# Optimization experiments

Measured on AMD Instinct MI355X. Metric: run time of the kernel, lower is better.

## Reference

```python
import jax, jax.numpy as jnp
import numpy as np

B, L, H, P = 4, 4096, 1024, 256


def _bin_op(ei, ej):
    A_i, Bu_i = ei
    A_j, Bu_j = ej
    return (A_j * A_i, A_j * Bu_i + Bu_j)


def _s5(x, log_real, imag, B_real, B_imag, C_real, C_imag, D, log_Delta):
    Lam = jax.lax.complex(-jnp.exp(log_real), imag)                 # [P]
    B_tilde = jax.lax.complex(B_real, B_imag)                        # [P,H]
    C_tilde = jax.lax.complex(C_real, C_imag)                        # [H,P]
    Delta = jnp.exp(log_Delta)                                       # [P]
    Lambda_bar = jnp.exp(Lam * Delta)                                # [P]
    Lam_safe = jnp.where(jnp.abs(Lam) < 1e-6,
                         jnp.full_like(Lam, 1e-6), Lam)
    B_bar = ((Lambda_bar - 1.0) / Lam_safe)[:, None] * B_tilde       # [P,H]
    Bu = x.astype(jnp.complex64) @ B_bar.T                           # [B,L,P]
    La = jnp.broadcast_to(Lambda_bar[None, None, :], Bu.shape)
    _, xs = jax.lax.associative_scan(_bin_op, (La, Bu), axis=1)      # [B,L,P]
    ys = jnp.real(xs @ C_tilde.T) + D * x                            # [B,L,H]
    return jax.nn.gelu(ys, approximate=False)


def setup_inputs() -> dict:
    key = jax.random.key(0)
    ks = jax.random.split(key, 17)
    std_b = 1.0 / H ** 0.5
    std_c = 1.0 / P ** 0.5
    d = {"x": jax.random.normal(ks[0], (B, L, H), dtype=jnp.float32)}
    for i, pfx in enumerate(["fwd", "bwd"]):
        o = 1 + 8 * i
        d[pfx + "_log_real"] = jax.random.normal(ks[o], (P,)) * 0.5
        d[pfx + "_imag"] = jax.random.normal(ks[o + 1], (P,))
        d[pfx + "_B_real"] = jax.random.normal(ks[o + 2], (P, H)) * std_b
        d[pfx + "_B_imag"] = jax.random.normal(ks[o + 3], (P, H)) * std_b
        d[pfx + "_C_real"] = jax.random.normal(ks[o + 4], (H, P)) * std_c
        d[pfx + "_C_imag"] = jax.random.normal(ks[o + 5], (H, P)) * std_c
        d[pfx + "_D"] = jnp.ones((H,), dtype=jnp.float32)
        d[pfx + "_log_Delta"] = jnp.zeros((P,), dtype=jnp.float32)
    return d


def reference(x,
              fwd_log_real, fwd_imag, fwd_B_real, fwd_B_imag,
              fwd_C_real, fwd_C_imag, fwd_D, fwd_log_Delta,
              bwd_log_real, bwd_imag, bwd_B_real, bwd_B_imag,
              bwd_C_real, bwd_C_imag, bwd_D, bwd_log_Delta):
    y_f = _s5(x, fwd_log_real, fwd_imag, fwd_B_real, fwd_B_imag,
              fwd_C_real, fwd_C_imag, fwd_D, fwd_log_Delta)
    x_flip = jnp.flip(x, axis=1)
    y_b = _s5(x_flip, bwd_log_real, bwd_imag, bwd_B_real, bwd_B_imag,
              bwd_C_real, bwd_C_imag, bwd_D, bwd_log_Delta)
    return y_f + jnp.flip(y_b, axis=1)
```

## Files before the change

kernel.cpp:

```cpp
#include <hip/hip_runtime.h>
#include <math.h>


typedef short bf16x8 __attribute__((ext_vector_type(8)));
typedef float f32x4 __attribute__((ext_vector_type(4)));
typedef unsigned short u16x8 __attribute__((ext_vector_type(8)));

__device__ __forceinline__ unsigned short f2bf(float f) {
  union { float f; unsigned int u; } v; v.f = f;
  unsigned int r = (v.u + 0x7FFFu + ((v.u >> 16) & 1u)) >> 16;
  return (unsigned short)r;
}
__device__ __forceinline__ float bf2f(unsigned short s) {
  union { unsigned int u; float f; } v; v.u = ((unsigned int)s) << 16;
  return v.f;
}
__device__ __forceinline__ float gelu_fast(float v) {
  const float u = 1.5957691216057308f * fmaf(0.044715f * v, v * v, v);
  return v / (1.f + __expf(-u));
}
__device__ __forceinline__ void gload16(const unsigned short* g, void* l) {
  __builtin_amdgcn_global_load_lds(
      (const __attribute__((address_space(1))) void*)g,
      (__attribute__((address_space(3))) void*)l, 16, 0, 0);
}

__global__ __launch_bounds__(256) void cast_x_kernel(
    const float* __restrict__ x, unsigned short* __restrict__ xbf) {
  const size_t i = (size_t)blockIdx.x * 256 + threadIdx.x;
  const float4* xv = (const float4*)x;
  float4 a = xv[2 * i], b = xv[2 * i + 1];
  u16x8 r;
  r[0] = f2bf(a.x); r[1] = f2bf(a.y); r[2] = f2bf(a.z); r[3] = f2bf(a.w);
  r[4] = f2bf(b.x); r[5] = f2bf(b.y); r[6] = f2bf(b.z); r[7] = f2bf(b.w);
  *(u16x8*)(xbf + 8 * i) = r;
}

__global__ __launch_bounds__(256) void prep_kernel(
    const float* __restrict__ flr, const float* __restrict__ fim,
    const float* __restrict__ fBr, const float* __restrict__ fBi,
    const float* __restrict__ fCr, const float* __restrict__ fCi,
    const float* __restrict__ flD,
    const float* __restrict__ blr, const float* __restrict__ bim,
    const float* __restrict__ bBr, const float* __restrict__ bBi,
    const float* __restrict__ bCr, const float* __restrict__ bCi,
    const float* __restrict__ blD,
    unsigned short* __restrict__ W, unsigned short* __restrict__ CmT,
    float4* __restrict__ lamp) {
  const int bid = blockIdx.x, tid = threadIdx.x;
  if (bid < 512) {
    const int dir = bid >> 8, p = bid & 255;
    const float* lr_ = dir ? blr : flr;
    const float* im_ = dir ? bim : fim;
    const float* lD_ = dir ? blD : flD;
    const float* Br_ = dir ? bBr : fBr;
    const float* Bi_ = dir ? bBi : fBi;
    const float Lre = -expf(lr_[p]);
    const float Lim = im_[p];
    const float Dl = expf(lD_[p]);
    const float ar = Lre * Dl, ai = Lim * Dl;
    const float er = expf(ar);
    const float lre = er * cosf(ai), lim = er * sinf(ai);
    const float e64 = expf(64.f * ar);
    const float l64re = e64 * cosf(64.f * ai), l64im = e64 * sinf(64.f * ai);
    float sre = Lre, sim = Lim;
    if (sqrtf(Lre * Lre + Lim * Lim) < 1e-6f) { sre = 1e-6f; sim = 0.f; }
    const float den = sre * sre + sim * sim;
    const float fre = ((lre - 1.f) * sre + lim * sim) / den;
    const float fi2 = (lim * sre - (lre - 1.f) * sim) / den;
    if (tid == 0) lamp[dir * 256 + p] = make_float4(lre, lim, l64re, l64im);
    const size_t rowR = (size_t)(dir * 512 + 2 * p) * 1024;
    const size_t rowI = rowR + 1024;
    for (int h = tid; h < 1024; h += 256) {
      const float Br = Br_[p * 1024 + h], Bi = Bi_[p * 1024 + h];
      W[rowR + h] = f2bf(fre * Br - fi2 * Bi);
      W[rowI + h] = f2bf(fre * Bi + fi2 * Br);
    }
  } else {
    const int h = bid - 512;
    for (int k = tid; k < 1024; k += 256) {
      const int dir = k >> 9, within = k & 511;
      const int p = within >> 1, comp = within & 1;
      const float* C = comp ? (dir ? bCi : fCi) : (dir ? bCr : fCr);
      float v = C[(size_t)h * 256 + p];
      if (comp) v = -v;
      CmT[(size_t)h * 1024 + k] = f2bf(v);
    }
  }
}

#define GEMM_KSTEP(ACC, KT, APTR, BPTR)                                        \
  {                                                                            \
    const int k0 = (KT) << 6;                                                  \
    _Pragma("unroll") for (int i = 0; i < 4; ++i) {                            \
      const int r = (i << 5) + tr;                                             \
      const int o = (i << 12) + (tid << 4);                                    \
      gload16(APTR + (size_t)(m0 + r) * 1024 + (k0 + csw), (char*)As + o);     \
      gload16(BPTR + (size_t)(n0 + r) * 1024 + (k0 + csw), (char*)Bs + o);     \
    }                                                                          \
    __syncthreads();                                                           \
    _Pragma("unroll") for (int kk = 0; kk < 64; kk += 32) {                    \
      bf16x8 af[4], bf_[4];                                                    \
      _Pragma("unroll") for (int m4 = 0; m4 < 4; ++m4) {                       \
        const int row = (wm << 6) + (m4 << 4) + fr;                            \
        af[m4] = *(const bf16x8*)&As[row * 64 + ((kk + ks) ^ sw)];             \
      }                                                                        \
      _Pragma("unroll") for (int n4 = 0; n4 < 4; ++n4) {                       \
        const int row = (wn << 6) + (n4 << 4) + fr;                            \
        bf_[n4] = *(const bf16x8*)&Bs[row * 64 + ((kk + ks) ^ sw)];            \
      }                                                                        \
      _Pragma("unroll") for (int m4 = 0; m4 < 4; ++m4)                         \
          _Pragma("unroll") for (int n4 = 0; n4 < 4; ++n4)                     \
              ACC[m4][n4] = __builtin_amdgcn_mfma_f32_16x16x32_bf16(           \
                  af[m4], bf_[n4], ACC[m4][n4], 0, 0, 0);                      \
    }                                                                          \
    __syncthreads();                                                           \
  }

__global__ __launch_bounds__(256) void gemm1_kernel(
    const unsigned short* __restrict__ xbf, const unsigned short* __restrict__ W,
    unsigned short* __restrict__ Zb) {
  __shared__ unsigned short As[128 * 64];
  __shared__ unsigned short Bs[128 * 64];
  const int tid = threadIdx.x;
  const int lane = tid & 63;
  const int w = tid >> 6;
  const int wm = w >> 1, wn = w & 1;
  const int fr = lane & 15;
  const int ks = (lane >> 4) << 3;
  const int sw = (fr & 7) << 3;
  const int tr = tid >> 3;
  const int csw = ((tid & 7) ^ (tr & 7)) << 3;
  const int bsw = ((blockIdx.x & 7) << 7) + (blockIdx.x >> 3);
  const int nt = bsw & 7, mt = bsw >> 3;
  const int m0 = mt << 7, n0 = nt << 7;

  f32x4 acc[4][4] = {};

  for (int kt = 0; kt < 16; ++kt) GEMM_KSTEP(acc, kt, xbf, W);

  const int rb = (lane >> 4) << 2;
#pragma unroll
  for (int m4 = 0; m4 < 4; ++m4)
#pragma unroll
    for (int n4 = 0; n4 < 4; ++n4) {
      const size_t gn = n0 + (wn << 6) + (n4 << 4) + fr;
#pragma unroll
      for (int r = 0; r < 4; ++r) {
        const size_t gm = m0 + (wm << 6) + (m4 << 4) + rb + r;
        Zb[gm * 1024 + gn] = f2bf(acc[m4][n4][r]);
      }
    }
}

__global__ __launch_bounds__(256) void scanA_kernel(
    unsigned int* __restrict__ Zp, const float4* __restrict__ lamp,
    float2* __restrict__ partials) {
  const int p = threadIdx.x;
  const int chunk = blockIdx.x & 63;
  const int dir = (blockIdx.x >> 6) & 1;
  const int b = blockIdx.x >> 7;
  const float4 lp = lamp[dir * 256 + p];
  const float lre = lp.x, lim = lp.y;
  const size_t col = (size_t)dir * 256 + p;
  const size_t mbase = (size_t)b * 4096 + (size_t)chunk * 64;
  float sre = 0.f, sim = 0.f;
  if (dir == 0) {
    for (int i = 0; i < 64; ++i) {
      const size_t idx = (mbase + i) * 512 + col;
      const unsigned int u = Zp[idx];
      const float ur = bf2f((unsigned short)u), ui = bf2f((unsigned short)(u >> 16));
      const float nr = fmaf(lre, sre, fmaf(-lim, sim, ur));
      const float ni = fmaf(lre, sim, fmaf(lim, sre, ui));
      sre = nr; sim = ni;
      Zp[idx] = (unsigned int)f2bf(sre) | ((unsigned int)f2bf(sim) << 16);
    }
  } else {
    for (int i = 63; i >= 0; --i) {
      const size_t idx = (mbase + i) * 512 + col;
      const unsigned int u = Zp[idx];
      const float ur = bf2f((unsigned short)u), ui = bf2f((unsigned short)(u >> 16));
      const float nr = fmaf(lre, sre, fmaf(-lim, sim, ur));
      const float ni = fmaf(lre, sim, fmaf(lim, sre, ui));
      sre = nr; sim = ni;
      Zp[idx] = (unsigned int)f2bf(sre) | ((unsigned int)f2bf(sim) << 16);
    }
  }
  partials[((size_t)(b * 2 + dir) * 256 + p) * 64 + chunk] = make_float2(sre, sim);
}

__global__ __launch_bounds__(256) void scanB_kernel(
    const float2* __restrict__ partials, float2* __restrict__ carries,
    const float4* __restrict__ lamp) {
  const int t = blockIdx.x * 256 + threadIdx.x;
  const int p = t & 255;
  const int dir = (t >> 8) & 1;
  const int b = t >> 9;
  const float4 lp = lamp[dir * 256 + p];
  const float ar = lp.z, ai = lp.w;
  const size_t base = ((size_t)(b * 2 + dir) * 256 + p) * 64;
  float cr = 0.f, ci = 0.f;
  if (dir == 0) {
    for (int c = 0; c < 64; ++c) {
      carries[base + c] = make_float2(cr, ci);
      float2 s = partials[base + c];
      float nr = fmaf(ar, cr, fmaf(-ai, ci, s.x));
      float ni = fmaf(ar, ci, fmaf(ai, cr, s.y));
      cr = nr; ci = ni;
    }
  } else {
    for (int c = 63; c >= 0; --c) {
      carries[base + c] = make_float2(cr, ci);
      float2 s = partials[base + c];
      float nr = fmaf(ar, cr, fmaf(-ai, ci, s.x));
      float ni = fmaf(ar, ci, fmaf(ai, cr, s.y));
      cr = nr; ci = ni;
    }
  }
}

__global__ __launch_bounds__(256) void scanC_kernel(
    const unsigned int* __restrict__ Zp, const float4* __restrict__ lamp,
    const float2* __restrict__ carries, unsigned int* __restrict__ xsbf) {
  const int p = threadIdx.x;
  const int chunk = blockIdx.x & 63;
  const int dir = (blockIdx.x >> 6) & 1;
  const int b = blockIdx.x >> 7;
  const float4 lp = lamp[dir * 256 + p];
  const float lre = lp.x, lim = lp.y;
  const size_t col = (size_t)dir * 256 + p;
  const size_t mbase = (size_t)b * 4096 + (size_t)chunk * 64;
  const float2 K = carries[((size_t)(b * 2 + dir) * 256 + p) * 64 + chunk];
  float qr = lre * K.x - lim * K.y;
  float qi = lre * K.y + lim * K.x;
  if (dir == 0) {
    for (int i = 0; i < 64; ++i) {
      const size_t idx = (mbase + i) * 512 + col;
      const unsigned int u = Zp[idx];
      const float vr = bf2f((unsigned short)u) + qr;
      const float vi = bf2f((unsigned short)(u >> 16)) + qi;
      xsbf[idx] = (unsigned int)f2bf(vr) | ((unsigned int)f2bf(vi) << 16);
      const float t2 = lre * qr - lim * qi;
      qi = lre * qi + lim * qr; qr = t2;
    }
  } else {
    for (int i = 63; i >= 0; --i) {
      const size_t idx = (mbase + i) * 512 + col;
      const unsigned int u = Zp[idx];
      const float vr = bf2f((unsigned short)u) + qr;
      const float vi = bf2f((unsigned short)(u >> 16)) + qi;
      xsbf[idx] = (unsigned int)f2bf(vr) | ((unsigned int)f2bf(vi) << 16);
      const float t2 = lre * qr - lim * qi;
      qi = lre * qi + lim * qr; qr = t2;
    }
  }
}

__global__ __launch_bounds__(256, 2) void gemm2_kernel(
    const unsigned short* __restrict__ A2, const unsigned short* __restrict__ CmT,
    const unsigned short* __restrict__ xbf, const float* __restrict__ Df,
    const float* __restrict__ Db, float* __restrict__ out) {
  __shared__ unsigned short As[128 * 64];
  __shared__ unsigned short Bs[128 * 64];
  const int tid = threadIdx.x;
  const int lane = tid & 63;
  const int w = tid >> 6;
  const int wm = w >> 1, wn = w & 1;
  const int fr = lane & 15;
  const int ks = (lane >> 4) << 3;
  const int sw = (fr & 7) << 3;
  const int tr = tid >> 3;
  const int csw = ((tid & 7) ^ (tr & 7)) << 3;
  const int bsw = ((blockIdx.x & 7) << 7) + (blockIdx.x >> 3);
  const int nt = bsw & 7, mt = bsw >> 3;
  const int m0 = mt << 7, n0 = nt << 7;

  f32x4 accf[4][4] = {};
  f32x4 accb[4][4] = {};

  for (int kt = 0; kt < 8; ++kt) GEMM_KSTEP(accf, kt, A2, CmT);
  for (int kt = 8; kt < 16; ++kt) GEMM_KSTEP(accb, kt, A2, CmT);

  const int rb = (lane >> 4) << 2;
#pragma unroll
  for (int n4 = 0; n4 < 4; ++n4) {
    const size_t gn = n0 + (wn << 6) + (n4 << 4) + fr;
    const float dfv = Df[gn], dbv = Db[gn];
#pragma unroll
    for (int m4 = 0; m4 < 4; ++m4) {
#pragma unroll
      for (int r = 0; r < 4; ++r) {
        const size_t gm = m0 + (wm << 6) + (m4 << 4) + rb + r;
        const float xv = bf2f(xbf[gm * 1024 + gn]);
        out[gm * 1024 + gn] = gelu_fast(accf[m4][n4][r] + dfv * xv) +
                              gelu_fast(accb[m4][n4][r] + dbv * xv);
      }
    }
  }
}

extern "C" void kernel_launch(void* const* d_in, const int* in_sizes, int n_in,
                              void* d_out, int out_size, void* d_ws, size_t ws_size,
                              hipStream_t stream) {
  const float* x = (const float*)d_in[0];
  const float* flr = (const float*)d_in[1];
  const float* fim = (const float*)d_in[2];
  const float* fBr = (const float*)d_in[3];
  const float* fBi = (const float*)d_in[4];
  const float* fCr = (const float*)d_in[5];
  const float* fCi = (const float*)d_in[6];
  const float* fD  = (const float*)d_in[7];
  const float* flD = (const float*)d_in[8];
  const float* blr = (const float*)d_in[9];
  const float* bim = (const float*)d_in[10];
  const float* bBr = (const float*)d_in[11];
  const float* bBi = (const float*)d_in[12];
  const float* bCr = (const float*)d_in[13];
  const float* bCi = (const float*)d_in[14];
  const float* bD  = (const float*)d_in[15];
  const float* blD = (const float*)d_in[16];

  char* ws = (char*)d_ws;
  unsigned short* xbf  = (unsigned short*)(ws);
  unsigned short* W    = (unsigned short*)(ws + 33554432);
  unsigned short* CmT  = (unsigned short*)(ws + 35651584);
  unsigned short* Zb   = (unsigned short*)(ws + 37748736);
  unsigned short* xsbf = (unsigned short*)(ws + 71303168);
  float4*         lamp = (float4*)(ws + 104857600);
  float2*         part = (float2*)(ws + 104865792);
  float2*         carr = (float2*)(ws + 105914368);

  dim3 blk(256);
  cast_x_kernel<<<8192, blk, 0, stream>>>(x, xbf);
  prep_kernel<<<1536, blk, 0, stream>>>(flr, fim, fBr, fBi, fCr, fCi, flD,
                                        blr, bim, bBr, bBi, bCr, bCi, blD,
                                        W, CmT, lamp);
  gemm1_kernel<<<1024, blk, 0, stream>>>(xbf, W, Zb);
  scanA_kernel<<<512, blk, 0, stream>>>((unsigned int*)Zb, lamp, part);
  scanB_kernel<<<8, blk, 0, stream>>>(part, carr, lamp);
  scanC_kernel<<<512, blk, 0, stream>>>((unsigned int*)Zb, lamp, carr,
                                        (unsigned int*)xsbf);
  gemm2_kernel<<<1024, blk, 0, stream>>>(xsbf, CmT, xbf, fD, bD, (float*)d_out);
}
```

Before: 162.9 us.

## Double-buffer LDS tiles in both GEMM kernels to overlap loads with MFMA

Splits the GEMM k-step into a stage (async global-to-LDS load) and a compute phase, with two LDS buffers per operand. The next k-tile is prefetched while MFMAs run on the current one, and one barrier per step replaces two. This hides global load latency but doubles LDS use to 64KB per block, which may reduce occupancy. It also relies on the async loads being complete at the single barrier, with no explicit wait on the load counter.

```diff
diff --git a/kernel.cpp b/kernel.cpp
--- a/kernel.cpp
+++ b/kernel.cpp
@@ -89,39 +89,42 @@
   }
 }
 
-#define GEMM_KSTEP(ACC, KT, APTR, BPTR)                                        \
+#define GEMM_STAGE(BUF, KT, APTR, BPTR)                                        \
   {                                                                            \
     const int k0 = (KT) << 6;                                                  \
     _Pragma("unroll") for (int i = 0; i < 4; ++i) {                            \
       const int r = (i << 5) + tr;                                             \
-      const int o = (i << 12) + (tid << 4);                                    \
+      const int o = ((BUF) << 14) + (i << 12) + (tid << 4);                    \
       gload16(APTR + (size_t)(m0 + r) * 1024 + (k0 + csw), (char*)As + o);     \
       gload16(BPTR + (size_t)(n0 + r) * 1024 + (k0 + csw), (char*)Bs + o);     \
     }                                                                          \
-    __syncthreads();                                                           \
+  }
+
+#define GEMM_COMPUTE(BUF, ACC)                                                 \
+  {                                                                            \
+    const int bo = (BUF) << 13;               \
     _Pragma("unroll") for (int kk = 0; kk < 64; kk += 32) {                    \
       bf16x8 af[4], bf_[4];                                                    \
       _Pragma("unroll") for (int m4 = 0; m4 < 4; ++m4) {                       \
         const int row = (wm << 6) + (m4 << 4) + fr;                            \
-        af[m4] = *(const bf16x8*)&As[row * 64 + ((kk + ks) ^ sw)];             \
+        af[m4] = *(const bf16x8*)&As[bo + row * 64 + ((kk + ks) ^ sw)];        \
       }                                                                        \
       _Pragma("unroll") for (int n4 = 0; n4 < 4; ++n4) {                       \
         const int row = (wn << 6) + (n4 << 4) + fr;                            \
-        bf_[n4] = *(const bf16x8*)&Bs[row * 64 + ((kk + ks) ^ sw)];            \
+        bf_[n4] = *(const bf16x8*)&Bs[bo + row * 64 + ((kk + ks) ^ sw)];       \
       }                                                                        \
       _Pragma("unroll") for (int m4 = 0; m4 < 4; ++m4)                         \
           _Pragma("unroll") for (int n4 = 0; n4 < 4; ++n4)                     \
               ACC[m4][n4] = __builtin_amdgcn_mfma_f32_16x16x32_bf16(           \
                   af[m4], bf_[n4], ACC[m4][n4], 0, 0, 0);                      \
     }                                                                          \
-    __syncthreads();                                                           \
   }
 
 __global__ __launch_bounds__(256) void gemm1_kernel(
     const unsigned short* __restrict__ xbf, const unsigned short* __restrict__ W,
     unsigned short* __restrict__ Zb) {
-  __shared__ unsigned short As[128 * 64];
-  __shared__ unsigned short Bs[128 * 64];
+  __shared__ unsigned short As[2 * 128 * 64];
+  __shared__ unsigned short Bs[2 * 128 * 64];
   const int tid = threadIdx.x;
   const int lane = tid & 63;
   const int w = tid >> 6;
@@ -137,7 +140,16 @@
 
   f32x4 acc[4][4] = {};
 
-  for (int kt = 0; kt < 16; ++kt) GEMM_KSTEP(acc, kt, xbf, W);
+  GEMM_STAGE(0, 0, xbf, W);
+  __syncthreads();
+  int cur = 0;
+  for (int kt = 0; kt < 15; ++kt) {
+    GEMM_STAGE(cur ^ 1, kt + 1, xbf, W);
+    GEMM_COMPUTE(cur, acc);
+    __syncthreads();
+    cur ^= 1;
+  }
+  GEMM_COMPUTE(cur, acc);
 
   const int rb = (lane >> 4) << 2;
 #pragma unroll
@@ -260,8 +272,8 @@
     const unsigned short* __restrict__ A2, const unsigned short* __restrict__ CmT,
     const unsigned short* __restrict__ xbf, const float* __restrict__ Df,
     const float* __restrict__ Db, float* __restrict__ out) {
-  __shared__ unsigned short As[128 * 64];
-  __shared__ unsigned short Bs[128 * 64];
+  __shared__ unsigned short As[2 * 128 * 64];
+  __shared__ unsigned short Bs[2 * 128 * 64];
   const int tid = threadIdx.x;
   const int lane = tid & 63;
   const int w = tid >> 6;
@@ -278,8 +290,23 @@
   f32x4 accf[4][4] = {};
   f32x4 accb[4][4] = {};
 
-  for (int kt = 0; kt < 8; ++kt) GEMM_KSTEP(accf, kt, A2, CmT);
-  for (int kt = 8; kt < 16; ++kt) GEMM_KSTEP(accb, kt, A2, CmT);
+  GEMM_STAGE(0, 0, A2, CmT);
+  __syncthreads();
+  int cur = 0;
+#pragma unroll
+  for (int kt = 0; kt < 8; ++kt) {
+    GEMM_STAGE(cur ^ 1, kt + 1, A2, CmT);
+    GEMM_COMPUTE(cur, accf);
+    __syncthreads();
+    cur ^= 1;
+  }
+#pragma unroll
+  for (int kt = 8; kt < 16; ++kt) {
+    if (kt < 15) GEMM_STAGE(cur ^ 1, kt + 1, A2, CmT);
+    GEMM_COMPUTE(cur, accb);
+    __syncthreads();
+    cur ^= 1;
+  }
 
   const int rb = (lane >> 4) << 2;
 #pragma unroll
```

New measurement: 185.7 us. +14.0%, slower.

## Fuse three-pass chunked scan into one kernel with flag-based cross-block carry exchange

Applied to the files above, without the earlier changes.

Replaces the scanA/scanB/scanC pipeline with a single kernel. Each block keeps its local scan results in registers, publishes its chunk total, waits on flags for all predecessor chunks, then sums their decayed totals to form its carry. This drops the write-back and re-read of Z, the separate carry kernel, and two launch boundaries. It relies on all 512 blocks being co-resident to avoid spin-wait deadlock, holds 64 registers per thread for the local buffer, and makes each block's carry computation O(k) in the number of preceding chunks.

```diff
diff --git a/kernel.cpp b/kernel.cpp
--- a/kernel.cpp
+++ b/kernel.cpp
@@ -34,6 +34,11 @@
   r[0] = f2bf(a.x); r[1] = f2bf(a.y); r[2] = f2bf(a.z); r[3] = f2bf(a.w);
   r[4] = f2bf(b.x); r[5] = f2bf(b.y); r[6] = f2bf(b.z); r[7] = f2bf(b.w);
   *(u16x8*)(xbf + 8 * i) = r;
+}
+
+__global__ __launch_bounds__(256) void clear_flags_kernel(
+    unsigned int* __restrict__ flags) {
+  flags[blockIdx.x * 256 + threadIdx.x] = 0u;
 }
 
 __global__ __launch_bounds__(256) void prep_kernel(
@@ -153,105 +158,103 @@
     }
 }
 
-__global__ __launch_bounds__(256) void scanA_kernel(
-    unsigned int* __restrict__ Zp, const float4* __restrict__ lamp,
-    float2* __restrict__ partials) {
+__global__ __launch_bounds__(256) void scan_fused_kernel(
+    const unsigned int* __restrict__ Zp, unsigned int* __restrict__ xsbf,
+    const float4* __restrict__ lamp, float2* __restrict__ part,
+    unsigned int* __restrict__ flags) {
   const int p = threadIdx.x;
-  const int chunk = blockIdx.x & 63;
-  const int dir = (blockIdx.x >> 6) & 1;
-  const int b = blockIdx.x >> 7;
+  const int k = blockIdx.x & 63;
+  const int s = blockIdx.x >> 6;
+  const int dir = s & 1, b = s >> 1;
   const float4 lp = lamp[dir * 256 + p];
-  const float lre = lp.x, lim = lp.y;
+  const float lre = lp.x, lim = lp.y, wr64 = lp.z, wi64 = lp.w;
   const size_t col = (size_t)dir * 256 + p;
-  const size_t mbase = (size_t)b * 4096 + (size_t)chunk * 64;
+  const size_t mbase = (size_t)b * 4096 + (size_t)k * 64;
+
+  unsigned int loc[64];
   float sre = 0.f, sim = 0.f;
   if (dir == 0) {
+#pragma unroll
     for (int i = 0; i < 64; ++i) {
-      const size_t idx = (mbase + i) * 512 + col;
-      const unsigned int u = Zp[idx];
-      const float ur = bf2f((unsigned short)u), ui = bf2f((unsigned short)(u >> 16));
-      const float nr = fmaf(lre, sre, fmaf(-lim, sim, ur));
-      const float ni = fmaf(lre, sim, fmaf(lim, sre, ui));
+      const unsigned int u = Zp[(mbase + i) * 512 + col];
+      const float nr = fmaf(lre, sre, fmaf(-lim, sim, bf2f((unsigned short)u)));
+      const float ni = fmaf(lre, sim, fmaf(lim, sre, bf2f((unsigned short)(u >> 16))));
       sre = nr; sim = ni;
-      Zp[idx] = (unsigned int)f2bf(sre) | ((unsigned int)f2bf(sim) << 16);
+      loc[i] = (unsigned int)f2bf(sre) | ((unsigned int)f2bf(sim) << 16);
     }
   } else {
+#pragma unroll
     for (int i = 63; i >= 0; --i) {
-      const size_t idx = (mbase + i) * 512 + col;
-      const unsigned int u = Zp[idx];
-      const float ur = bf2f((unsigned short)u), ui = bf2f((unsigned short)(u >> 16));
-      const float nr = fmaf(lre, sre, fmaf(-lim, sim, ur));
-      const float ni = fmaf(lre, sim, fmaf(lim, sre, ui));
+      const unsigned int u = Zp[(mbase + i) * 512 + col];
+      const float nr = fmaf(lre, sre, fmaf(-lim, sim, bf2f((unsigned short)u)));
+      const float ni = fmaf(lre, sim, fmaf(lim, sre, bf2f((unsigned short)(u >> 16))));
       sre = nr; sim = ni;
-      Zp[idx] = (unsigned int)f2bf(sre) | ((unsigned int)f2bf(sim) << 16);
-    }
-  }
-  partials[((size_t)(b * 2 + dir) * 256 + p) * 64 + chunk] = make_float2(sre, sim);
-}
-
-__global__ __launch_bounds__(256) void scanB_kernel(
-    const float2* __restrict__ partials, float2* __restrict__ carries,
-    const float4* __restrict__ lamp) {
-  const int t = blockIdx.x * 256 + threadIdx.x;
-  const int p = t & 255;
-  const int dir = (t >> 8) & 1;
-  const int b = t >> 9;
-  const float4 lp = lamp[dir * 256 + p];
-  const float ar = lp.z, ai = lp.w;
-  const size_t base = ((size_t)(b * 2 + dir) * 256 + p) * 64;
-  float cr = 0.f, ci = 0.f;
+      loc[i] = (unsigned int)f2bf(sre) | ((unsigned int)f2bf(sim) << 16);
+    }
+  }
+
+  part[(size_t)(s * 64 + k) * 256 + p] = make_float2(sre, sim);
+  __syncthreads();
+  if (p == 0) {
+    __threadfence();
+    __hip_atomic_store(&flags[s * 64 + k], 1u, __ATOMIC_RELEASE,
+                       __HIP_MEMORY_SCOPE_AGENT);
+    if (dir == 0) {
+      for (int j = 0; j < k; ++j)
+        while (__hip_atomic_load(&flags[s * 64 + j], __ATOMIC_ACQUIRE,
+                                 __HIP_MEMORY_SCOPE_AGENT) == 0u)
+          __builtin_amdgcn_s_sleep(8);
+    } else {
+      for (int j = k + 1; j < 64; ++j)
+        while (__hip_atomic_load(&flags[s * 64 + j], __ATOMIC_ACQUIRE,
+                                 __HIP_MEMORY_SCOPE_AGENT) == 0u)
+          __builtin_amdgcn_s_sleep(8);
+    }
+  }
+  __syncthreads();
+
+  float cr = 0.f, ci = 0.f, wr = 1.f, wi = 0.f;
   if (dir == 0) {
-    for (int c = 0; c < 64; ++c) {
-      carries[base + c] = make_float2(cr, ci);
-      float2 s = partials[base + c];
-      float nr = fmaf(ar, cr, fmaf(-ai, ci, s.x));
-      float ni = fmaf(ar, ci, fmaf(ai, cr, s.y));
-      cr = nr; ci = ni;
+    for (int j = k - 1; j >= 0; --j) {
+      const float2 S = part[(size_t)(s * 64 + j) * 256 + p];
+      cr = fmaf(wr, S.x, fmaf(-wi, S.y, cr));
+      ci = fmaf(wr, S.y, fmaf(wi, S.x, ci));
+      const float t = wr * wr64 - wi * wi64;
+      wi = wr * wi64 + wi * wr64; wr = t;
     }
   } else {
-    for (int c = 63; c >= 0; --c) {
-      carries[base + c] = make_float2(cr, ci);
-      float2 s = partials[base + c];
-      float nr = fmaf(ar, cr, fmaf(-ai, ci, s.x));
-      float ni = fmaf(ar, ci, fmaf(ai, cr, s.y));
-      cr = nr; ci = ni;
-    }
-  }
-}
-
-__global__ __launch_bounds__(256) void scanC_kernel(
-    const unsigned int* __restrict__ Zp, const float4* __restrict__ lamp,
-    const float2* __restrict__ carries, unsigned int* __restrict__ xsbf) {
-  const int p = threadIdx.x;
-  const int chunk = blockIdx.x & 63;
-  const int dir = (blockIdx.x >> 6) & 1;
-  const int b = blockIdx.x >> 7;
-  const float4 lp = lamp[dir * 256 + p];
-  const float lre = lp.x, lim = lp.y;
-  const size_t col = (size_t)dir * 256 + p;
-  const size_t mbase = (size_t)b * 4096 + (size_t)chunk * 64;
-  const float2 K = carries[((size_t)(b * 2 + dir) * 256 + p) * 64 + chunk];
-  float qr = lre * K.x - lim * K.y;
-  float qi = lre * K.y + lim * K.x;
+    for (int j = k + 1; j < 64; ++j) {
+      const float2 S = part[(size_t)(s * 64 + j) * 256 + p];
+      cr = fmaf(wr, S.x, fmaf(-wi, S.y, cr));
+      ci = fmaf(wr, S.y, fmaf(wi, S.x, ci));
+      const float t = wr * wr64 - wi * wi64;
+      wi = wr * wi64 + wi * wr64; wr = t;
+    }
+  }
+
+  float qr = lre * cr - lim * ci;
+  float qi = lre * ci + lim * cr;
   if (dir == 0) {
+#pragma unroll
     for (int i = 0; i < 64; ++i) {
-      const size_t idx = (mbase + i) * 512 + col;
-      const unsigned int u = Zp[idx];
+      const unsigned int u = loc[i];
       const float vr = bf2f((unsigned short)u) + qr;
       const float vi = bf2f((unsigned short)(u >> 16)) + qi;
-      xsbf[idx] = (unsigned int)f2bf(vr) | ((unsigned int)f2bf(vi) << 16);
-      const float t2 = lre * qr - lim * qi;
-      qi = lre * qi + lim * qr; qr = t2;
+      xsbf[(mbase + i) * 512 + col] =
+          (unsigned int)f2bf(vr) | ((unsigned int)f2bf(vi) << 16);
+      const float t = lre * qr - lim * qi;
+      qi = lre * qi + lim * qr; qr = t;
     }
   } else {
+#pragma unroll
     for (int i = 63; i >= 0; --i) {
-      const size_t idx = (mbase + i) * 512 + col;
-      const unsigned int u = Zp[idx];
+      const unsigned int u = loc[i];
       const float vr = bf2f((unsigned short)u) + qr;
       const float vi = bf2f((unsigned short)(u >> 16)) + qi;
-      xsbf[idx] = (unsigned int)f2bf(vr) | ((unsigned int)f2bf(vi) << 16);
-      const float t2 = lre * qr - lim * qi;
-      qi = lre * qi + lim * qr; qr = t2;
+      xsbf[(mbase + i) * 512 + col] =
+          (unsigned int)f2bf(vr) | ((unsigned int)f2bf(vi) << 16);
+      const float t = lre * qr - lim * qi;
+      qi = lre * qi + lim * qr; qr = t;
     }
   }
 }
@@ -328,17 +331,17 @@
   unsigned short* xsbf = (unsigned short*)(ws + 71303168);
   float4*         lamp = (float4*)(ws + 104857600);
   float2*         part = (float2*)(ws + 104865792);
-  float2*         carr = (float2*)(ws + 105914368);
+  unsigned int*   flgs = (unsigned int*)(ws + 105914368);
 
   dim3 blk(256);
   cast_x_kernel<<<8192, blk, 0, stream>>>(x, xbf);
+  clear_flags_kernel<<<2, blk, 0, stream>>>(flgs);
   prep_kernel<<<1536, blk, 0, stream>>>(flr, fim, fBr, fBi, fCr, fCi, flD,
                                         blr, bim, bBr, bBi, bCr, bCi, blD,
                                         W, CmT, lamp);
   gemm1_kernel<<<1024, blk, 0, stream>>>(xbf, W, Zb);
-  scanA_kernel<<<512, blk, 0, stream>>>((unsigned int*)Zb, lamp, part);
-  scanB_kernel<<<8, blk, 0, stream>>>(part, carr, lamp);
-  scanC_kernel<<<512, blk, 0, stream>>>((unsigned int*)Zb, lamp, carr,
-                                        (unsigned int*)xsbf);
+  scan_fused_kernel<<<512, blk, 0, stream>>>((unsigned int*)Zb,
+                                             (unsigned int*)xsbf, lamp, part,
+                                             flgs);
   gemm2_kernel<<<1024, blk, 0, stream>>>(xsbf, CmT, xbf, fD, bD, (float*)d_out);
 }
```

After: 279.6 us. +71.7%, slower.
